# Optimization experiments

Hardware: AMD Instinct MI355X
Metric: run time of the kernel (lower is better)

Reference implementation:

```python
import jax, jax.numpy as jnp
import numpy as np

# Conv2D_DT config (matches init_kwargs)
IN_C = 64
OUT_C = 128
K = (3, 3)
STRIDE = (1, 1)
PAD = (1, 1)
DIL = (1, 1)
INPUT_DIM = K[0] * K[1] * IN_C  # 576


def setup_inputs() -> dict:
    key = jax.random.key(0)
    k1, k2 = jax.random.split(key)
    x = jax.random.normal(k1, (32, IN_C, 56, 56), dtype=jnp.float32)
    # DistanceTransform centroids: one INPUT_DIM-dim center per output channel
    W = jax.random.normal(k2, (OUT_C, INPUT_DIM), dtype=jnp.float32) * (1.0 / np.sqrt(INPUT_DIM))
    return {"x": x, "W": W}


def _unfold_patches(x):
    # Equivalent of nn.Unfold: output [N, C*kH*kW, oH, oW], feature dim ordered
    # (channel, kh, kw) — matches torch.nn.Unfold ordering.
    return jax.lax.conv_general_dilated_patches(
        x,
        filter_shape=K,
        window_strides=STRIDE,
        padding=[(PAD[0], PAD[0]), (PAD[1], PAD[1])],
        rhs_dilation=DIL,
        dimension_numbers=("NCHW", "OIHW", "NCHW"),
    )


def reference(x, W):
    # patches: [N, D, oH, oW] with D = C*kH*kW
    patches = _unfold_patches(x)
    # Euclidean (p=2) distance between every patch and every centroid, via the
    # expanded quadratic form (the compute-heavy cross term is a GEMM):
    # ||p - w||^2 = ||p||^2 + ||w||^2 - 2 p.w
    x2 = jnp.sum(patches * patches, axis=1)            # [N, oH, oW]
    w2 = jnp.sum(W * W, axis=1)                        # [O]
    cross = jnp.einsum("ndhw,od->nohw", patches, W)    # [N, O, oH, oW]
    d2 = x2[:, None] + w2[None, :, None, None] - 2.0 * cross
    dist = jnp.sqrt(jnp.maximum(d2, 0.0))              # [N, O, oH, oW]
    return dist
```

## Files before the change

### kernel.cpp

```cpp
#include <hip/hip_runtime.h>
#include <hip/hip_bf16.h>
#include <stdint.h>
#include <math.h>

#define NIMG 32
#define CIN 64
#define HWD 56
#define OCH 128
#define PH 58

typedef __attribute__((ext_vector_type(8))) short bfrag;
typedef __attribute__((ext_vector_type(4))) float facc;
typedef __attribute__((ext_vector_type(8))) unsigned short u16x8;

__device__ __forceinline__ unsigned short f2bf(float f) {
  union { float f; uint32_t u; } a; a.f = f;
  uint32_t u = a.u;
  return (unsigned short)((u + 0x7FFFu + ((u >> 16) & 1u)) >> 16);
}

__device__ __forceinline__ void gload_lds16(const void* g, void* l) {
  __builtin_amdgcn_global_load_lds(
      (const __attribute__((address_space(1))) unsigned int*)g,
      (__attribute__((address_space(3))) unsigned int*)l, 16, 0, 0);
}

__global__ __launch_bounds__(256) void k_prep_x(const float* __restrict__ x,
                                                unsigned short* __restrict__ xh,
                                                float* __restrict__ s) {
  const int n = blockIdx.x / HWD, h = blockIdx.x % HWD;
  __shared__ float xt[CIN][HWD + 1];
  const float* xp = x + ((size_t)n * CIN * HWD + h) * HWD;
  for (int i = threadIdx.x; i < CIN * HWD; i += 256) {
    int c = i / HWD, ww = i % HWD;
    xt[c][ww] = xp[(size_t)c * HWD * HWD + ww];
  }
  __syncthreads();
  const size_t rowbase = ((size_t)(n * PH + h + 1) * PH + 1) * CIN;
  for (int t = threadIdx.x; t < HWD * 8; t += 256) {
    int ww = t >> 3, seg = t & 7;
    u16x8 v;
#pragma unroll
    for (int j = 0; j < 8; ++j) v[j] = f2bf(xt[seg * 8 + j][ww]);
    *(u16x8*)(xh + rowbase + (size_t)ww * CIN + seg * 8) = v;
  }
  for (int ww = threadIdx.x; ww < HWD; ww += 256) {
    float acc = 0.f;
#pragma unroll
    for (int c = 0; c < CIN; ++c) { float v = xt[c][ww]; acc += v * v; }
    s[((size_t)n * HWD + h) * HWD + ww] = acc;
  }
  if (threadIdx.x < 16) {
    int ww = (threadIdx.x >> 3) ? (PH - 1) : 0, seg = threadIdx.x & 7;
    u16x8 z = {0, 0, 0, 0, 0, 0, 0, 0};
    *(u16x8*)(xh + ((size_t)(n * PH + h + 1) * PH + ww) * CIN + seg * 8) = z;
  }
  if (h == 0) {
    u16x8 z = {0, 0, 0, 0, 0, 0, 0, 0};
    for (int t = threadIdx.x; t < 2 * PH * 8; t += 256) {
      int r = (t >= PH * 8) ? (PH - 1) : 0;
      int rem = t % (PH * 8);
      int ww = rem >> 3, seg = rem & 7;
      *(u16x8*)(xh + ((size_t)(n * PH + r) * PH + ww) * CIN + seg * 8) = z;
    }
  }
}

__global__ __launch_bounds__(256) void k_x2(const float* __restrict__ s,
                                            float* __restrict__ x2) {
  int i = blockIdx.x * 256 + threadIdx.x;
  if (i >= NIMG * HWD * HWD) return;
  int n = i / (HWD * HWD), r = i % (HWD * HWD), oh = r / HWD, ow = r % HWD;
  const float* sp = s + (size_t)n * HWD * HWD;
  float acc = 0.f;
#pragma unroll
  for (int dh = -1; dh <= 1; ++dh) {
    int hh = oh + dh;
    if ((unsigned)hh >= HWD) continue;
#pragma unroll
    for (int dw = -1; dw <= 1; ++dw) {
      int wwp = ow + dw;
      if ((unsigned)wwp >= HWD) continue;
      acc += sp[hh * HWD + wwp];
    }
  }
  x2[i] = acc;
}

__global__ __launch_bounds__(64) void k_prep_w(const float* __restrict__ W,
                                               unsigned short* __restrict__ Wt,
                                               float* __restrict__ w2) {
  int o = blockIdx.x, c = threadIdx.x;
  float sum = 0.f;
#pragma unroll
  for (int kp = 0; kp < 9; ++kp) {
    float v = W[o * 576 + c * 9 + kp];
    sum += v * v;
    Wt[(size_t)kp * (OCH * CIN) + o * CIN + c] = f2bf(v);
  }
#pragma unroll
  for (int off = 32; off; off >>= 1) sum += __shfl_down(sum, off);
  if (c == 0) w2[o] = sum;
}

__global__ __launch_bounds__(256, 2) void k_main(
    const unsigned short* __restrict__ xh, const unsigned short* __restrict__ Wt,
    const float* __restrict__ x2, const float* __restrict__ w2,
    float* __restrict__ out) {
  __shared__ __align__(16) unsigned short slab[352 * 64];
  const int bid = blockIdx.x;
  const int n = bid / 14, band = bid % 14;
  const int oh0 = band * 4;
  const int tid = threadIdx.x, wv = tid >> 6, lane = tid & 63;

  {
    const int seg = lane & 7, r8 = lane >> 3;
    for (int i = wv; i < 44; i += 4) {
      int row = i * 8 + r8;
      int re = row < 348 ? row : 347;
      int lseg = seg ^ (re & 7);
      int dr = re / 58, pc = re % 58;
      const unsigned short* src =
          xh + ((size_t)(n * PH + oh0 + dr) * PH + pc) * CIN + lseg * 8;
      gload_lds16(src, (char*)slab + i * 1024);
    }
  }
  __syncthreads();

  const int lane15 = lane & 15, q = lane >> 4;
  const int wm = wv >> 1, wn = wv & 1;

  int srow0[7];
#pragma unroll
  for (int mf = 0; mf < 7; ++mf) {
    int pl = wm * 112 + mf * 16 + lane15;
    srow0[mf] = (pl / 56) * 58 + (pl % 56);
  }
  int boff[4];
#pragma unroll
  for (int nf = 0; nf < 4; ++nf)
    boff[nf] = (wn * 64 + nf * 16 + lane15) * CIN + q * 8;

  facc acc[7][4] = {};

  const char* slabb = (const char*)slab;
  for (int kh = 0; kh < 3; ++kh) {
    for (int kw = 0; kw < 3; ++kw) {
      const unsigned short* wtk = Wt + (size_t)(kh * 3 + kw) * (OCH * CIN);
#pragma unroll
      for (int cs = 0; cs < 2; ++cs) {
        const int cbyte = cs * 64 + q * 16;
        bfrag a[7];
#pragma unroll
        for (int mf = 0; mf < 7; ++mf) {
          int srow = srow0[mf] + kh * 58 + kw;
          a[mf] = *(const bfrag*)(slabb + srow * 128 + (cbyte ^ ((srow & 7) << 4)));
        }
#pragma unroll
        for (int nf = 0; nf < 4; ++nf) {
          bfrag b = *(const bfrag*)(wtk + boff[nf] + cs * 32);
#pragma unroll
          for (int mf = 0; mf < 7; ++mf)
            acc[mf][nf] =
                __builtin_amdgcn_mfma_f32_16x16x32_bf16(a[mf], b, acc[mf][nf], 0, 0, 0);
        }
      }
    }
  }

#pragma unroll
  for (int mf = 0; mf < 7; ++mf) {
    int mb = wm * 112 + mf * 16 + q * 4;
    int oh = oh0 + mb / 56, ow = mb % 56;
    facc xv = *(const facc*)(x2 + ((size_t)n * HWD + oh) * HWD + ow);
#pragma unroll
    for (int nf = 0; nf < 4; ++nf) {
      int o = wn * 64 + nf * 16 + lane15;
      float w2o = w2[o];
      facc d;
#pragma unroll
      for (int r = 0; r < 4; ++r) {
        float v = xv[r] + w2o - 2.0f * acc[mf][nf][r];
        d[r] = sqrtf(v > 0.f ? v : 0.f);
      }
      *(facc*)(out + (((size_t)n * OCH + o) * HWD + oh) * HWD + ow) = d;
    }
  }
}

extern "C" void kernel_launch(void* const* d_in, const int* in_sizes, int n_in,
                              void* d_out, int out_size, void* d_ws, size_t ws_size,
                              hipStream_t stream) {
  const float* x = (const float*)d_in[0];
  const float* W = (const float*)d_in[1];
  float* out = (float*)d_out;
  char* ws = (char*)d_ws;

  unsigned short* xh = (unsigned short*)ws;
  float* s = (float*)(ws + 13778944);
  float* x2 = (float*)(ws + 13778944 + 401408);
  unsigned short* Wt = (unsigned short*)(ws + 13778944 + 802816);
  float* w2 = (float*)(ws + 13778944 + 802816 + 147456);

  k_prep_x<<<dim3(NIMG * HWD), dim3(256), 0, stream>>>(x, xh, s);
  k_x2<<<dim3((NIMG * HWD * HWD + 255) / 256), dim3(256), 0, stream>>>(s, x2);
  k_prep_w<<<dim3(OCH), dim3(64), 0, stream>>>(W, Wt, w2);
  k_main<<<dim3(NIMG * 14), dim3(256), 0, stream>>>(xh, Wt, x2, w2, out);
}
```

Measured before the change: 122.2 us.

## Retile main kernel to 8x8 spatial blocks and merge aux prep kernels

The main GEMM kernel now tiles output into 8x8 spatial patches per block (1568 blocks) instead of 4-row bands (448 blocks). This shrinks the LDS slab and the accumulator registers, which allows higher occupancy (launch bounds 4), and fully unrolls the kh/kw loops. The x2 and weight-prep kernels are merged into one launch to save a launch. The trade-off is a larger halo fraction per tile: 100 rows loaded for 64 outputs instead of 348 for 224. Each wave also issues fewer MFMAs per B-fragment load, so weight loads are reused less.

```diff
diff --git a/kernel.cpp b/kernel.cpp
--- a/kernel.cpp
+++ b/kernel.cpp
@@ -66,62 +66,64 @@
   }
 }
 
-__global__ __launch_bounds__(256) void k_x2(const float* __restrict__ s,
-                                            float* __restrict__ x2) {
-  int i = blockIdx.x * 256 + threadIdx.x;
-  if (i >= NIMG * HWD * HWD) return;
-  int n = i / (HWD * HWD), r = i % (HWD * HWD), oh = r / HWD, ow = r % HWD;
-  const float* sp = s + (size_t)n * HWD * HWD;
-  float acc = 0.f;
-#pragma unroll
-  for (int dh = -1; dh <= 1; ++dh) {
-    int hh = oh + dh;
-    if ((unsigned)hh >= HWD) continue;
-#pragma unroll
-    for (int dw = -1; dw <= 1; ++dw) {
-      int wwp = ow + dw;
-      if ((unsigned)wwp >= HWD) continue;
-      acc += sp[hh * HWD + wwp];
-    }
-  }
-  x2[i] = acc;
-}
-
-__global__ __launch_bounds__(64) void k_prep_w(const float* __restrict__ W,
-                                               unsigned short* __restrict__ Wt,
-                                               float* __restrict__ w2) {
-  int o = blockIdx.x, c = threadIdx.x;
-  float sum = 0.f;
-#pragma unroll
-  for (int kp = 0; kp < 9; ++kp) {
-    float v = W[o * 576 + c * 9 + kp];
-    sum += v * v;
-    Wt[(size_t)kp * (OCH * CIN) + o * CIN + c] = f2bf(v);
-  }
-#pragma unroll
-  for (int off = 32; off; off >>= 1) sum += __shfl_down(sum, off);
-  if (c == 0) w2[o] = sum;
-}
-
-__global__ __launch_bounds__(256, 2) void k_main(
+__global__ __launch_bounds__(256) void k_aux(const float* __restrict__ s,
+                                             float* __restrict__ x2,
+                                             const float* __restrict__ W,
+                                             unsigned short* __restrict__ Wt,
+                                             float* __restrict__ w2) {
+  if (blockIdx.x < 392) {
+    int i = blockIdx.x * 256 + threadIdx.x;
+    if (i >= NIMG * HWD * HWD) return;
+    int n = i / (HWD * HWD), r = i % (HWD * HWD), oh = r / HWD, ow = r % HWD;
+    const float* sp = s + (size_t)n * HWD * HWD;
+    float acc = 0.f;
+#pragma unroll
+    for (int dh = -1; dh <= 1; ++dh) {
+      int hh = oh + dh;
+      if ((unsigned)hh >= HWD) continue;
+#pragma unroll
+      for (int dw = -1; dw <= 1; ++dw) {
+        int wwp = ow + dw;
+        if ((unsigned)wwp >= HWD) continue;
+        acc += sp[hh * HWD + wwp];
+      }
+    }
+    x2[i] = acc;
+  } else {
+    if (threadIdx.x >= 64) return;
+    int o = blockIdx.x - 392, c = threadIdx.x;
+    float sum = 0.f;
+#pragma unroll
+    for (int kp = 0; kp < 9; ++kp) {
+      float v = W[o * 576 + c * 9 + kp];
+      sum += v * v;
+      Wt[(size_t)kp * (OCH * CIN) + o * CIN + c] = f2bf(v);
+    }
+#pragma unroll
+    for (int off = 32; off; off >>= 1) sum += __shfl_down(sum, off);
+    if (c == 0) w2[o] = sum;
+  }
+}
+
+__global__ __launch_bounds__(256, 4) void k_main(
     const unsigned short* __restrict__ xh, const unsigned short* __restrict__ Wt,
     const float* __restrict__ x2, const float* __restrict__ w2,
     float* __restrict__ out) {
-  __shared__ __align__(16) unsigned short slab[352 * 64];
+  __shared__ __align__(16) unsigned short slab[104 * 64];
   const int bid = blockIdx.x;
-  const int n = bid / 14, band = bid % 14;
-  const int oh0 = band * 4;
+  const int n = bid / 49, t49 = bid % 49;
+  const int oh0 = (t49 / 7) * 8, ow0 = (t49 % 7) * 8;
   const int tid = threadIdx.x, wv = tid >> 6, lane = tid & 63;
 
   {
     const int seg = lane & 7, r8 = lane >> 3;
-    for (int i = wv; i < 44; i += 4) {
+    for (int i = wv; i < 13; i += 4) {
       int row = i * 8 + r8;
-      int re = row < 348 ? row : 347;
+      int re = row < 100 ? row : 99;
       int lseg = seg ^ (re & 7);
-      int dr = re / 58, pc = re % 58;
+      int dr = re / 10, dc = re % 10;
       const unsigned short* src =
-          xh + ((size_t)(n * PH + oh0 + dr) * PH + pc) * CIN + lseg * 8;
+          xh + ((size_t)(n * PH + oh0 + dr) * PH + (ow0 + dc)) * CIN + lseg * 8;
       gload_lds16(src, (char*)slab + i * 1024);
     }
   }
@@ -130,37 +132,39 @@
   const int lane15 = lane & 15, q = lane >> 4;
   const int wm = wv >> 1, wn = wv & 1;
 
-  int srow0[7];
-#pragma unroll
-  for (int mf = 0; mf < 7; ++mf) {
-    int pl = wm * 112 + mf * 16 + lane15;
-    srow0[mf] = (pl / 56) * 58 + (pl % 56);
+  int srow0[2];
+#pragma unroll
+  for (int mf = 0; mf < 2; ++mf) {
+    int m = wm * 32 + mf * 16 + lane15;
+    srow0[mf] = (m >> 3) * 10 + (m & 7);
   }
   int boff[4];
 #pragma unroll
   for (int nf = 0; nf < 4; ++nf)
     boff[nf] = (wn * 64 + nf * 16 + lane15) * CIN + q * 8;
 
-  facc acc[7][4] = {};
+  facc acc[2][4] = {};
 
   const char* slabb = (const char*)slab;
+#pragma unroll
   for (int kh = 0; kh < 3; ++kh) {
+#pragma unroll
     for (int kw = 0; kw < 3; ++kw) {
       const unsigned short* wtk = Wt + (size_t)(kh * 3 + kw) * (OCH * CIN);
 #pragma unroll
       for (int cs = 0; cs < 2; ++cs) {
         const int cbyte = cs * 64 + q * 16;
-        bfrag a[7];
-#pragma unroll
-        for (int mf = 0; mf < 7; ++mf) {
-          int srow = srow0[mf] + kh * 58 + kw;
+        bfrag a[2];
+#pragma unroll
+        for (int mf = 0; mf < 2; ++mf) {
+          int srow = srow0[mf] + kh * 10 + kw;
           a[mf] = *(const bfrag*)(slabb + srow * 128 + (cbyte ^ ((srow & 7) << 4)));
         }
 #pragma unroll
         for (int nf = 0; nf < 4; ++nf) {
           bfrag b = *(const bfrag*)(wtk + boff[nf] + cs * 32);
 #pragma unroll
-          for (int mf = 0; mf < 7; ++mf)
+          for (int mf = 0; mf < 2; ++mf)
             acc[mf][nf] =
                 __builtin_amdgcn_mfma_f32_16x16x32_bf16(a[mf], b, acc[mf][nf], 0, 0, 0);
         }
@@ -169,9 +173,10 @@
   }
 
 #pragma unroll
-  for (int mf = 0; mf < 7; ++mf) {
-    int mb = wm * 112 + mf * 16 + q * 4;
-    int oh = oh0 + mb / 56, ow = mb % 56;
+  for (int mf = 0; mf < 2; ++mf) {
+    int mb = wm * 32 + mf * 16 + q * 4;
+    int dh = mb >> 3, dw0 = mb & 7;
+    int oh = oh0 + dh, ow = ow0 + dw0;
     facc xv = *(const facc*)(x2 + ((size_t)n * HWD + oh) * HWD + ow);
 #pragma unroll
     for (int nf = 0; nf < 4; ++nf) {
@@ -203,7 +208,6 @@
   float* w2 = (float*)(ws + 13778944 + 802816 + 147456);
 
   k_prep_x<<<dim3(NIMG * HWD), dim3(256), 0, stream>>>(x, xh, s);
-  k_x2<<<dim3((NIMG * HWD * HWD + 255) / 256), dim3(256), 0, stream>>>(s, x2);
-  k_prep_w<<<dim3(OCH), dim3(64), 0, stream>>>(W, Wt, w2);
-  k_main<<<dim3(NIMG * 14), dim3(256), 0, stream>>>(xh, Wt, x2, w2, out);
-}
+  k_aux<<<dim3(392 + OCH), dim3(256), 0, stream>>>(s, x2, W, Wt, w2);
+  k_main<<<dim3(NIMG * 49), dim3(256), 0, stream>>>(xh, Wt, x2, w2, out);
+}
```

After: 163.0 us. 33.4% more time.

## Double-buffer MFMA operand loads and merge x2/weight prep kernels

Applied to the files above, without the earlier changes.

The main GEMM loop is flattened into 18 k-steps, and the A (LDS) and B (global) fragments for the next step are loaded into a second register buffer while the MFMAs of the current step run, so load latency is hidden. The separate x2 stencil kernel and weight-prep kernel are merged into one launch, with block ranges dispatching to each task, which removes one kernel launch. Double buffering doubles the fragment registers (22 more bfrags) under a launch bound of 2 blocks per SM, which risks spilling or lower occupancy.

```diff
diff --git a/kernel.cpp b/kernel.cpp
--- a/kernel.cpp
+++ b/kernel.cpp
@@ -66,41 +66,43 @@
   }
 }
 
-__global__ __launch_bounds__(256) void k_x2(const float* __restrict__ s,
-                                            float* __restrict__ x2) {
-  int i = blockIdx.x * 256 + threadIdx.x;
-  if (i >= NIMG * HWD * HWD) return;
-  int n = i / (HWD * HWD), r = i % (HWD * HWD), oh = r / HWD, ow = r % HWD;
-  const float* sp = s + (size_t)n * HWD * HWD;
-  float acc = 0.f;
-#pragma unroll
-  for (int dh = -1; dh <= 1; ++dh) {
-    int hh = oh + dh;
-    if ((unsigned)hh >= HWD) continue;
-#pragma unroll
-    for (int dw = -1; dw <= 1; ++dw) {
-      int wwp = ow + dw;
-      if ((unsigned)wwp >= HWD) continue;
-      acc += sp[hh * HWD + wwp];
-    }
-  }
-  x2[i] = acc;
-}
-
-__global__ __launch_bounds__(64) void k_prep_w(const float* __restrict__ W,
-                                               unsigned short* __restrict__ Wt,
-                                               float* __restrict__ w2) {
-  int o = blockIdx.x, c = threadIdx.x;
-  float sum = 0.f;
-#pragma unroll
-  for (int kp = 0; kp < 9; ++kp) {
-    float v = W[o * 576 + c * 9 + kp];
-    sum += v * v;
-    Wt[(size_t)kp * (OCH * CIN) + o * CIN + c] = f2bf(v);
-  }
-#pragma unroll
-  for (int off = 32; off; off >>= 1) sum += __shfl_down(sum, off);
-  if (c == 0) w2[o] = sum;
+__global__ __launch_bounds__(256) void k_aux(const float* __restrict__ s,
+                                             float* __restrict__ x2,
+                                             const float* __restrict__ W,
+                                             unsigned short* __restrict__ Wt,
+                                             float* __restrict__ w2) {
+  if (blockIdx.x < 392) {
+    int i = blockIdx.x * 256 + threadIdx.x;
+    if (i >= NIMG * HWD * HWD) return;
+    int n = i / (HWD * HWD), r = i % (HWD * HWD), oh = r / HWD, ow = r % HWD;
+    const float* sp = s + (size_t)n * HWD * HWD;
+    float acc = 0.f;
+#pragma unroll
+    for (int dh = -1; dh <= 1; ++dh) {
+      int hh = oh + dh;
+      if ((unsigned)hh >= HWD) continue;
+#pragma unroll
+      for (int dw = -1; dw <= 1; ++dw) {
+        int wwp = ow + dw;
+        if ((unsigned)wwp >= HWD) continue;
+        acc += sp[hh * HWD + wwp];
+      }
+    }
+    x2[i] = acc;
+  } else {
+    if (threadIdx.x >= 64) return;
+    int o = blockIdx.x - 392, c = threadIdx.x;
+    float sum = 0.f;
+#pragma unroll
+    for (int kp = 0; kp < 9; ++kp) {
+      float v = W[o * 576 + c * 9 + kp];
+      sum += v * v;
+      Wt[(size_t)kp * (OCH * CIN) + o * CIN + c] = f2bf(v);
+    }
+#pragma unroll
+    for (int off = 32; off; off >>= 1) sum += __shfl_down(sum, off);
+    if (c == 0) w2[o] = sum;
+  }
 }
 
 __global__ __launch_bounds__(256, 2) void k_main(
@@ -127,7 +129,7 @@
   }
   __syncthreads();
 
-  const int lane15 = lane & 15, q = lane >> 4;
+  const int lane15 = lane & 15, q = lane >> 4, q16 = q * 16;
   const int wm = wv >> 1, wn = wv & 1;
 
   int srow0[7];
@@ -141,31 +143,40 @@
   for (int nf = 0; nf < 4; ++nf)
     boff[nf] = (wn * 64 + nf * 16 + lane15) * CIN + q * 8;
 
+  const char* slabb = (const char*)slab;
+
+  auto load_b = [&](bfrag* dst, int ks) {
+    const unsigned short* wp = Wt + (size_t)(ks >> 1) * (OCH * CIN) + (ks & 1) * 32;
+#pragma unroll
+    for (int nf = 0; nf < 4; ++nf) dst[nf] = *(const bfrag*)(wp + boff[nf]);
+  };
+  auto load_a = [&](bfrag* dst, int ks) {
+    const int kp = ks >> 1, cbyte = (ks & 1) * 64 + q16;
+    const int rof = (kp / 3) * 58 + (kp % 3);
+#pragma unroll
+    for (int mf = 0; mf < 7; ++mf) {
+      int srow = srow0[mf] + rof;
+      dst[mf] = *(const bfrag*)(slabb + srow * 128 + (cbyte ^ ((srow & 7) << 4)));
+    }
+  };
+
   facc acc[7][4] = {};
-
-  const char* slabb = (const char*)slab;
-  for (int kh = 0; kh < 3; ++kh) {
-    for (int kw = 0; kw < 3; ++kw) {
-      const unsigned short* wtk = Wt + (size_t)(kh * 3 + kw) * (OCH * CIN);
-#pragma unroll
-      for (int cs = 0; cs < 2; ++cs) {
-        const int cbyte = cs * 64 + q * 16;
-        bfrag a[7];
-#pragma unroll
-        for (int mf = 0; mf < 7; ++mf) {
-          int srow = srow0[mf] + kh * 58 + kw;
-          a[mf] = *(const bfrag*)(slabb + srow * 128 + (cbyte ^ ((srow & 7) << 4)));
-        }
-#pragma unroll
-        for (int nf = 0; nf < 4; ++nf) {
-          bfrag b = *(const bfrag*)(wtk + boff[nf] + cs * 32);
-#pragma unroll
-          for (int mf = 0; mf < 7; ++mf)
-            acc[mf][nf] =
-                __builtin_amdgcn_mfma_f32_16x16x32_bf16(a[mf], b, acc[mf][nf], 0, 0, 0);
-        }
-      }
-    }
+  bfrag a[2][7], b[2][4];
+  load_b(b[0], 0);
+  load_a(a[0], 0);
+#pragma unroll
+  for (int ks = 0; ks < 18; ++ks) {
+    const int cur = ks & 1, nxt = cur ^ 1;
+    if (ks < 17) {
+      load_b(b[nxt], ks + 1);
+      load_a(a[nxt], ks + 1);
+    }
+#pragma unroll
+    for (int nf = 0; nf < 4; ++nf)
+#pragma unroll
+      for (int mf = 0; mf < 7; ++mf)
+        acc[mf][nf] = __builtin_amdgcn_mfma_f32_16x16x32_bf16(a[cur][mf], b[cur][nf],
+                                                              acc[mf][nf], 0, 0, 0);
   }
 
 #pragma unroll
@@ -203,7 +214,6 @@
   float* w2 = (float*)(ws + 13778944 + 802816 + 147456);
 
   k_prep_x<<<dim3(NIMG * HWD), dim3(256), 0, stream>>>(x, xh, s);
-  k_x2<<<dim3((NIMG * HWD * HWD + 255) / 256), dim3(256), 0, stream>>>(s, x2);
-  k_prep_w<<<dim3(OCH), dim3(64), 0, stream>>>(W, Wt, w2);
+  k_aux<<<dim3(392 + OCH), dim3(256), 0, stream>>>(s, x2, W, Wt, w2);
   k_main<<<dim3(NIMG * 14), dim3(256), 0, stream>>>(xh, Wt, x2, w2, out);
 }
```

Result: no change. 120.5 us (-1.4%).
